# Optimization experiments

Measured on AMD Instinct MI355X. Metric: run time of the kernel, lower is better.

Reference implementation:

```python
import jax, jax.numpy as jnp
import numpy as np

H = 768
L = 4096
P, KP = 8192, 8
EV, KE = 2048, 6
E = 16384
NR = 32
NUM_LABELS = 2


def setup_inputs() -> dict:
    key = jax.random.key(0)
    ks = jax.random.split(key, 10)
    seq = jax.random.normal(ks[0], (1, L, H), dtype=jnp.float32)
    phrase_idx = jax.random.randint(ks[1], (P, KP), 0, L, dtype=jnp.int32)
    phrase_mask = jnp.ones((P, KP), dtype=jnp.float32)
    event_idx = jax.random.randint(ks[2], (EV, KE), 0, L, dtype=jnp.int32)
    event_mask = jnp.ones((EV, KE), dtype=jnp.float32)
    pair_idx = jax.random.randint(ks[3], (E, 2), 0, EV, dtype=jnp.int32)
    root_idx = jax.random.randint(ks[4], (NR,), 0, P, dtype=jnp.int32)
    s1 = 1.0 / np.sqrt(2 * H)
    W1 = jax.random.normal(ks[5], (2 * H, H), dtype=jnp.float32) * s1
    b1 = jnp.zeros((H,), dtype=jnp.float32)
    Wb = jax.random.normal(ks[6], (2 * H, NUM_LABELS), dtype=jnp.float32) * s1
    bb = jnp.zeros((NUM_LABELS,), dtype=jnp.float32)
    return {"seq": seq, "phrase_idx": phrase_idx, "phrase_mask": phrase_mask,
            "event_idx": event_idx, "event_mask": event_mask, "pair_idx": pair_idx,
            "root_idx": root_idx, "W1": W1, "b1": b1, "Wb": Wb, "bb": bb}


def _masked_mean_gather(tok, idx, mask):
    # tok: [L,H]; idx: [N,K] int; mask: [N,K] float -> [N,H]
    g = tok[idx]                                  # [N,K,H] irregular gather
    s = jnp.einsum('nkh,nk->nh', g, mask)
    d = jnp.maximum(mask.sum(axis=1, keepdims=True), 1.0)
    return s / d


def reference(seq, phrase_idx, phrase_mask, event_idx, event_mask, pair_idx,
              root_idx, W1, b1, Wb, bb):
    tok = seq[0]                                   # [L,H] doc token embeddings
    # phrase embeddings: gather token indices per phrase, masked mean-pool
    ph = _masked_mean_gather(tok, phrase_idx, phrase_mask)   # [P,H]
    # event embeddings: gather span tokens per event, masked mean-pool
    ev = _masked_mean_gather(tok, event_idx, event_mask)     # [EV,H]
    # event-pair nodes: concat the two event embeddings, middle_layer MLP
    e1 = ev[pair_idx[:, 0]]                        # [E,H]
    e2 = ev[pair_idx[:, 1]]                        # [E,H]
    pairs = jnp.concatenate([e1, e2], axis=-1)     # [E,2H]
    node = jax.nn.relu(pairs @ W1 + b1)            # [E,H] (dropout inactive at eval)
    # virtual root: mean of sentence-root phrase embeddings
    vroot = ph[root_idx].mean(axis=0)              # [H]
    feat = jnp.concatenate([node, jnp.broadcast_to(vroot, node.shape)], axis=-1)
    logits = feat @ Wb + bb                        # [E,NUM_LABELS] bilinear classifier
    return logits
```

## Files before the change

### kernel.cpp

```cpp
#include <hip/hip_runtime.h>
#include <hip/hip_bf16.h>

#define H   768
#define H4  192
#define EVN 2048
#define KE  6
#define KP  8
#define EE  16384
#define NR  32

typedef __bf16 v8bf __attribute__((ext_vector_type(8)));
typedef float  v4f  __attribute__((ext_vector_type(4)));

__device__ __forceinline__ void gload16(const void* g, void* lds) {
    __builtin_amdgcn_global_load_lds(
        (const __attribute__((address_space(1))) void*)g,
        (__attribute__((address_space(3))) void*)lds, 16, 0, 0);
}
__device__ __forceinline__ float blo(unsigned u) {
    return __uint_as_float(u << 16);
}
__device__ __forceinline__ float bhi(unsigned u) {
    return __uint_as_float(u & 0xffff0000u);
}

__global__ __launch_bounds__(256) void pre_kernel(
    const float* __restrict__ seq,
    const int* __restrict__ eidx, const float* __restrict__ emask,
    const int* __restrict__ pidx, const float* __restrict__ pmask,
    const int* __restrict__ root_idx, const float* __restrict__ W1,
    const float* __restrict__ Wb,
    __hip_bfloat16* __restrict__ evb, __hip_bfloat16* __restrict__ Wt,
    float* __restrict__ dotr) {
    __shared__ float tile[64][65];
    const int b = blockIdx.x;
    const int t = threadIdx.x;
    const float4* seq4 = (const float4*)seq;

    if (b < 512) {
        const int w = t >> 6, l = t & 63;
        const int n = b * 4 + w;
        int idx[KE]; float mk[KE]; float ms = 0.f;
#pragma unroll
        for (int k = 0; k < KE; ++k) {
            idx[k] = eidx[n * KE + k];
            mk[k]  = emask[n * KE + k];
            ms    += mk[k];
        }
        const float inv = 1.f / fmaxf(ms, 1.f);
#pragma unroll
        for (int g = 0; g < 3; ++g) {
            const int t4 = l + g * 64;
            float4 acc = {0.f, 0.f, 0.f, 0.f};
#pragma unroll
            for (int k = 0; k < KE; ++k) {
                float4 v = seq4[idx[k] * H4 + t4];
                acc.x = fmaf(mk[k], v.x, acc.x);
                acc.y = fmaf(mk[k], v.y, acc.y);
                acc.z = fmaf(mk[k], v.z, acc.z);
                acc.w = fmaf(mk[k], v.w, acc.w);
            }
            __hip_bfloat16 o[4];
            o[0] = __float2bfloat16(acc.x * inv);
            o[1] = __float2bfloat16(acc.y * inv);
            o[2] = __float2bfloat16(acc.z * inv);
            o[3] = __float2bfloat16(acc.w * inv);
            *(uint2*)&evb[n * H + t4 * 4] = *(uint2*)o;
        }
    } else if (b < 520) {
        const int w = t >> 6, l = t & 63;
        const int r = (b - 512) * 4 + w;
        const int pr = root_idx[r];
        int idx[KP]; float mk[KP]; float ms = 0.f;
#pragma unroll
        for (int k = 0; k < KP; ++k) {
            idx[k] = pidx[pr * KP + k];
            mk[k]  = pmask[pr * KP + k];
            ms    += mk[k];
        }
        const float inv = 1.f / fmaxf(ms, 1.f);
        float p0 = 0.f, p1 = 0.f;
#pragma unroll
        for (int g = 0; g < 3; ++g) {
            const int t4 = l + g * 64;
            float4 a = {0.f, 0.f, 0.f, 0.f};
#pragma unroll
            for (int k = 0; k < KP; ++k) {
                float4 v = seq4[idx[k] * H4 + t4];
                a.x = fmaf(mk[k], v.x, a.x);
                a.y = fmaf(mk[k], v.y, a.y);
                a.z = fmaf(mk[k], v.z, a.z);
                a.w = fmaf(mk[k], v.w, a.w);
            }
            const int d = t4 * 4;
            float4 q0 = *(const float4*)&Wb[(H + d) * 2];
            float4 q1 = *(const float4*)&Wb[(H + d) * 2 + 4];
            p0 += inv * (a.x * q0.x + a.y * q0.z + a.z * q1.x + a.w * q1.z);
            p1 += inv * (a.x * q0.y + a.y * q0.w + a.z * q1.y + a.w * q1.w);
        }
#pragma unroll
        for (int off = 32; off > 0; off >>= 1) {
            p0 += __shfl_xor(p0, off, 64);
            p1 += __shfl_xor(p1, off, 64);
        }
        if (l == 0) {
            dotr[r * 2 + 0] = p0 * (1.0f / NR);
            dotr[r * 2 + 1] = p1 * (1.0f / NR);
        }
    } else {
        const int b2 = b - 520;
        const int k0 = (b2 % 12) * 64;
        const int j0 = (b2 / 12) * 64;
        const int s  = (j0 >= H) ? H : 0;
        const int n0 = j0 - s;
        const int c  = t & 63;
        const int r0 = t >> 6;
#pragma unroll
        for (int i = 0; i < 16; ++i) {
            const int r = r0 + i * 4;
            tile[r][c] = W1[(size_t)(s + k0 + r) * H + n0 + c];
        }
        __syncthreads();
#pragma unroll
        for (int i = 0; i < 16; ++i) {
            const int r = r0 + i * 4;
            Wt[(size_t)(j0 + r) * H + k0 + c] = __float2bfloat16(tile[c][r]);
        }
    }
}

__global__ __launch_bounds__(256) void gemm_kernel(
    const __hip_bfloat16* __restrict__ evb_,
    const __hip_bfloat16* __restrict__ Wt_,
    const float* __restrict__ b1v,
    __hip_bfloat16* __restrict__ evw) {
    __shared__ short As[3][8192];
    __shared__ short Bs[3][6144];

    const short* evb = (const short*)evb_;
    const short* Wt  = (const short*)Wt_;

    const int bid = blockIdx.x;
    const int swz = (bid & 7) * 32 + (bid >> 3);
    const int mt = swz >> 4, nt = swz & 15;
    const int m0 = mt * 128, n0 = nt * 96;

    const int t = threadIdx.x;
    const int l = t & 63;
    const int w = t >> 6;
    const int wr = (w >> 1) * 64;
    const int wc = (w & 1) * 48;

    const short* aSrc[4]; int aOff[4];
#pragma unroll
    for (int c = 0; c < 4; ++c) {
        const int s = c * 256 + t;
        const int r = s >> 3, pg = s & 7, g = pg ^ (r & 7);
        aSrc[c] = evb + (size_t)(m0 + r) * H + g * 8;
        aOff[c] = s * 16;
    }
    const short* bSrc[3]; int bOff[3];
#pragma unroll
    for (int c = 0; c < 3; ++c) {
        const int s = c * 256 + t;
        const int r = s >> 3, pg = s & 7, g = pg ^ (r & 7);
        bSrc[c] = Wt + (size_t)(n0 + r) * H + g * 8;
        bOff[c] = s * 16;
    }

#define STAGE(tile, buf) do {                                              \
    _Pragma("unroll") for (int c_ = 0; c_ < 4; ++c_)                       \
        gload16(aSrc[c_] + (tile) * 64, (char*)As[buf] + aOff[c_]);        \
    _Pragma("unroll") for (int c_ = 0; c_ < 3; ++c_)                       \
        gload16(bSrc[c_] + (tile) * 64, (char*)Bs[buf] + bOff[c_]);        \
} while (0)

    const int fr = l & 15, gq = l >> 4, xm = fr & 7;
    int aRowB[4], bRowB[3];
#pragma unroll
    for (int mi = 0; mi < 4; ++mi) aRowB[mi] = (wr + mi * 16 + fr) * 128;
#pragma unroll
    for (int nj = 0; nj < 3; ++nj) bRowB[nj] = (wc + nj * 16 + fr) * 128;

    v4f acc[4][3] = {};

    STAGE(0, 0);
    STAGE(1, 1);

#pragma unroll
    for (int ks = 0; ks < 12; ++ks) {
        if (ks < 11) { asm volatile("s_waitcnt vmcnt(7)" ::: "memory"); }
        else         { asm volatile("s_waitcnt vmcnt(0)" ::: "memory"); }
        __builtin_amdgcn_sched_barrier(0);
        __builtin_amdgcn_s_barrier();
        __builtin_amdgcn_sched_barrier(0);
        if (ks < 10) STAGE(ks + 2, (ks + 2) % 3);
        const char* Ab = (const char*)As[ks % 3];
        const char* Bb = (const char*)Bs[ks % 3];
#pragma unroll
        for (int hh = 0; hh < 2; ++hh) {
            const int pgo = ((hh * 4 + gq) ^ xm) * 16;
            v8bf a0 = *(const v8bf*)(Ab + aRowB[0] + pgo);
            v8bf a1 = *(const v8bf*)(Ab + aRowB[1] + pgo);
            v8bf a2 = *(const v8bf*)(Ab + aRowB[2] + pgo);
            v8bf a3 = *(const v8bf*)(Ab + aRowB[3] + pgo);
            v8bf b0 = *(const v8bf*)(Bb + bRowB[0] + pgo);
            v8bf b1 = *(const v8bf*)(Bb + bRowB[1] + pgo);
            v8bf b2 = *(const v8bf*)(Bb + bRowB[2] + pgo);
            acc[0][0] = __builtin_amdgcn_mfma_f32_16x16x32_bf16(a0, b0, acc[0][0], 0, 0, 0);
            acc[0][1] = __builtin_amdgcn_mfma_f32_16x16x32_bf16(a0, b1, acc[0][1], 0, 0, 0);
            acc[0][2] = __builtin_amdgcn_mfma_f32_16x16x32_bf16(a0, b2, acc[0][2], 0, 0, 0);
            acc[1][0] = __builtin_amdgcn_mfma_f32_16x16x32_bf16(a1, b0, acc[1][0], 0, 0, 0);
            acc[1][1] = __builtin_amdgcn_mfma_f32_16x16x32_bf16(a1, b1, acc[1][1], 0, 0, 0);
            acc[1][2] = __builtin_amdgcn_mfma_f32_16x16x32_bf16(a1, b2, acc[1][2], 0, 0, 0);
            acc[2][0] = __builtin_amdgcn_mfma_f32_16x16x32_bf16(a2, b0, acc[2][0], 0, 0, 0);
            acc[2][1] = __builtin_amdgcn_mfma_f32_16x16x32_bf16(a2, b1, acc[2][1], 0, 0, 0);
            acc[2][2] = __builtin_amdgcn_mfma_f32_16x16x32_bf16(a2, b2, acc[2][2], 0, 0, 0);
            acc[3][0] = __builtin_amdgcn_mfma_f32_16x16x32_bf16(a3, b0, acc[3][0], 0, 0, 0);
            acc[3][1] = __builtin_amdgcn_mfma_f32_16x16x32_bf16(a3, b1, acc[3][1], 0, 0, 0);
            acc[3][2] = __builtin_amdgcn_mfma_f32_16x16x32_bf16(a3, b2, acc[3][2], 0, 0, 0);
        }
    }
#undef STAGE

    float bv[3];
#pragma unroll
    for (int nj = 0; nj < 3; ++nj) {
        const int ocol = n0 + wc + nj * 16 + fr;
        bv[nj] = (ocol >= H) ? b1v[ocol - H] : 0.f;
    }
#pragma unroll
    for (int mi = 0; mi < 4; ++mi)
#pragma unroll
        for (int nj = 0; nj < 3; ++nj) {
            const int ocol = n0 + wc + nj * 16 + fr;
#pragma unroll
            for (int r = 0; r < 4; ++r) {
                const int orow = m0 + wr + mi * 16 + gq * 4 + r;
                evw[(size_t)orow * 1536 + ocol] =
                    __float2bfloat16(acc[mi][nj][r] + bv[nj]);
            }
        }
}

__global__ __launch_bounds__(256) void pair_logits_kernel(
    const __hip_bfloat16* __restrict__ evw_, const int* __restrict__ pair_idx,
    const float* __restrict__ Wb, const float* __restrict__ dotr,
    const float* __restrict__ bbv, float* __restrict__ out) {
    const ushort* evw = (const ushort*)evw_;
    const int wave = threadIdx.x >> 6;
    const int lane = threadIdx.x & 63;

    float c0 = 0.f, c1 = 0.f;
    if (lane < 32) { c0 = dotr[lane * 2]; c1 = dotr[lane * 2 + 1]; }
#pragma unroll
    for (int off = 32; off > 0; off >>= 1) {
        c0 += __shfl_xor(c0, off, 64);
        c1 += __shfl_xor(c1, off, 64);
    }
    c0 += bbv[0]; c1 += bbv[1];

    const int i = blockIdx.x * 4 + wave;
    const int p0 = pair_idx[i * 2 + 0];
    const int p1 = pair_idx[i * 2 + 1];
    const ushort* ra = evw + (size_t)p0 * 1536;
    const ushort* rb = evw + (size_t)p1 * 1536 + H;
    float acc0 = 0.f, acc1 = 0.f;
#pragma unroll
    for (int h = 0; h < 2; ++h) {
        const int j = h * 384 + lane * 6;
        uint3 ua = *(const uint3*)(ra + j);
        uint3 ub = *(const uint3*)(rb + j);
        float4 w0 = *(const float4*)(Wb + j * 2);
        float4 w1 = *(const float4*)(Wb + j * 2 + 4);
        float4 w2 = *(const float4*)(Wb + j * 2 + 8);
        float n0 = fmaxf(blo(ua.x) + blo(ub.x), 0.f);
        float n1 = fmaxf(bhi(ua.x) + bhi(ub.x), 0.f);
        float n2 = fmaxf(blo(ua.y) + blo(ub.y), 0.f);
        float n3 = fmaxf(bhi(ua.y) + bhi(ub.y), 0.f);
        float n4 = fmaxf(blo(ua.z) + blo(ub.z), 0.f);
        float n5 = fmaxf(bhi(ua.z) + bhi(ub.z), 0.f);
        acc0 += n0 * w0.x + n1 * w0.z + n2 * w1.x + n3 * w1.z + n4 * w2.x + n5 * w2.z;
        acc1 += n0 * w0.y + n1 * w0.w + n2 * w1.y + n3 * w1.w + n4 * w2.y + n5 * w2.w;
    }
#pragma unroll
    for (int off = 32; off > 0; off >>= 1) {
        acc0 += __shfl_xor(acc0, off, 64);
        acc1 += __shfl_xor(acc1, off, 64);
    }
    if (lane == 0) {
        out[i * 2 + 0] = acc0 + c0;
        out[i * 2 + 1] = acc1 + c1;
    }
}

extern "C" void kernel_launch(void* const* d_in, const int* in_sizes, int n_in,
                              void* d_out, int out_size, void* d_ws, size_t ws_size,
                              hipStream_t stream) {
    const float* seq         = (const float*)d_in[0];
    const int*   phrase_idx  = (const int*)  d_in[1];
    const float* phrase_mask = (const float*)d_in[2];
    const int*   event_idx   = (const int*)  d_in[3];
    const float* event_mask  = (const float*)d_in[4];
    const int*   pair_idx    = (const int*)  d_in[5];
    const int*   root_idx    = (const int*)  d_in[6];
    const float* W1          = (const float*)d_in[7];
    const float* b1          = (const float*)d_in[8];
    const float* Wb          = (const float*)d_in[9];
    const float* bb          = (const float*)d_in[10];
    float* out = (float*)d_out;

    char* wsb = (char*)d_ws;
    __hip_bfloat16* evb = (__hip_bfloat16*)wsb;
    __hip_bfloat16* Wt  = (__hip_bfloat16*)(wsb + 3145728);
    __hip_bfloat16* evw = (__hip_bfloat16*)(wsb + 5505024);
    float* dotr = (float*)(wsb + 11796480);

    pre_kernel<<<808, 256, 0, stream>>>(seq, event_idx, event_mask,
                                        phrase_idx, phrase_mask, root_idx,
                                        W1, Wb, evb, Wt, dotr);
    gemm_kernel<<<256, 256, 0, stream>>>(evb, Wt, b1, evw);
    pair_logits_kernel<<<EE / 4, 256, 0, stream>>>(evw, pair_idx, Wb, dotr,
                                                   bb, out);
}
```

Before: 33.89 us.

## Load GEMM B operand directly to registers and shrink N tile to 64

The GEMM stops staging the weight tile through LDS. Each wave now loads its B fragments straight from global memory into double-buffered registers one k-step ahead. The N tile drops from 96 to 64 columns, so the grid grows from 256 to 384 blocks with a new swizzle, and the vmcnt wait counts are adjusted to match. This removes LDS traffic and shared memory for B and raises block count for better CU coverage, at the cost of uncoalesced, redundant per-wave global reads of B and less reuse of A per block.

```diff
diff --git a/kernel.cpp b/kernel.cpp
--- a/kernel.cpp
+++ b/kernel.cpp
@@ -135,21 +135,20 @@
     const float* __restrict__ b1v,
     __hip_bfloat16* __restrict__ evw) {
     __shared__ short As[3][8192];
-    __shared__ short Bs[3][6144];
 
     const short* evb = (const short*)evb_;
     const short* Wt  = (const short*)Wt_;
 
     const int bid = blockIdx.x;
-    const int swz = (bid & 7) * 32 + (bid >> 3);
-    const int mt = swz >> 4, nt = swz & 15;
-    const int m0 = mt * 128, n0 = nt * 96;
+    const int swz = (bid & 7) * 48 + (bid >> 3);
+    const int mt = swz / 24, nt = swz % 24;
+    const int m0 = mt * 128, n0 = nt * 64;
 
     const int t = threadIdx.x;
     const int l = t & 63;
     const int w = t >> 6;
     const int wr = (w >> 1) * 64;
-    const int wc = (w & 1) * 48;
+    const int wc = (w & 1) * 32;
 
     const short* aSrc[4]; int aOff[4];
 #pragma unroll
@@ -159,44 +158,53 @@
         aSrc[c] = evb + (size_t)(m0 + r) * H + g * 8;
         aOff[c] = s * 16;
     }
-    const short* bSrc[3]; int bOff[3];
-#pragma unroll
-    for (int c = 0; c < 3; ++c) {
-        const int s = c * 256 + t;
-        const int r = s >> 3, pg = s & 7, g = pg ^ (r & 7);
-        bSrc[c] = Wt + (size_t)(n0 + r) * H + g * 8;
-        bOff[c] = s * 16;
-    }
-
-#define STAGE(tile, buf) do {                                              \
+
+#define STAGEA(tile, buf) do {                                             \
     _Pragma("unroll") for (int c_ = 0; c_ < 4; ++c_)                       \
         gload16(aSrc[c_] + (tile) * 64, (char*)As[buf] + aOff[c_]);        \
-    _Pragma("unroll") for (int c_ = 0; c_ < 3; ++c_)                       \
-        gload16(bSrc[c_] + (tile) * 64, (char*)Bs[buf] + bOff[c_]);        \
 } while (0)
 
     const int fr = l & 15, gq = l >> 4, xm = fr & 7;
-    int aRowB[4], bRowB[3];
+    int aRowB[4];
 #pragma unroll
     for (int mi = 0; mi < 4; ++mi) aRowB[mi] = (wr + mi * 16 + fr) * 128;
-#pragma unroll
-    for (int nj = 0; nj < 3; ++nj) bRowB[nj] = (wc + nj * 16 + fr) * 128;
-
-    v4f acc[4][3] = {};
-
-    STAGE(0, 0);
-    STAGE(1, 1);
+
+    const short* bPtr[2];
+#pragma unroll
+    for (int nj = 0; nj < 2; ++nj)
+        bPtr[nj] = Wt + (size_t)(n0 + wc + nj * 16 + fr) * H + gq * 8;
+
+    v8bf bS0[2][2], bS1[2][2];
+
+#define LOADB0(ks) do {                                                    \
+    _Pragma("unroll") for (int nj_ = 0; nj_ < 2; ++nj_)                    \
+        _Pragma("unroll") for (int hh_ = 0; hh_ < 2; ++hh_)                \
+            bS0[nj_][hh_] =                                                \
+                *(const v8bf*)(bPtr[nj_] + (ks) * 64 + hh_ * 32);          \
+} while (0)
+#define LOADB1(ks) do {                                                    \
+    _Pragma("unroll") for (int nj_ = 0; nj_ < 2; ++nj_)                    \
+        _Pragma("unroll") for (int hh_ = 0; hh_ < 2; ++hh_)                \
+            bS1[nj_][hh_] =                                                \
+                *(const v8bf*)(bPtr[nj_] + (ks) * 64 + hh_ * 32);          \
+} while (0)
+
+    v4f acc[4][2] = {};
+
+    LOADB0(0);
+    STAGEA(0, 0);
+    STAGEA(1, 1);
 
 #pragma unroll
     for (int ks = 0; ks < 12; ++ks) {
-        if (ks < 11) { asm volatile("s_waitcnt vmcnt(7)" ::: "memory"); }
+        if (ks < 11) { asm volatile("s_waitcnt vmcnt(4)" ::: "memory"); }
         else         { asm volatile("s_waitcnt vmcnt(0)" ::: "memory"); }
         __builtin_amdgcn_sched_barrier(0);
         __builtin_amdgcn_s_barrier();
         __builtin_amdgcn_sched_barrier(0);
-        if (ks < 10) STAGE(ks + 2, (ks + 2) % 3);
+        if (ks < 11) { if (ks & 1) LOADB0(ks + 1); else LOADB1(ks + 1); }
+        if (ks < 10) STAGEA(ks + 2, (ks + 2) % 3);
         const char* Ab = (const char*)As[ks % 3];
-        const char* Bb = (const char*)Bs[ks % 3];
 #pragma unroll
         for (int hh = 0; hh < 2; ++hh) {
             const int pgo = ((hh * 4 + gq) ^ xm) * 16;
@@ -204,35 +212,32 @@
             v8bf a1 = *(const v8bf*)(Ab + aRowB[1] + pgo);
             v8bf a2 = *(const v8bf*)(Ab + aRowB[2] + pgo);
             v8bf a3 = *(const v8bf*)(Ab + aRowB[3] + pgo);
-            v8bf b0 = *(const v8bf*)(Bb + bRowB[0] + pgo);
-            v8bf b1 = *(const v8bf*)(Bb + bRowB[1] + pgo);
-            v8bf b2 = *(const v8bf*)(Bb + bRowB[2] + pgo);
+            v8bf b0 = (ks & 1) ? bS1[0][hh] : bS0[0][hh];
+            v8bf b1 = (ks & 1) ? bS1[1][hh] : bS0[1][hh];
             acc[0][0] = __builtin_amdgcn_mfma_f32_16x16x32_bf16(a0, b0, acc[0][0], 0, 0, 0);
             acc[0][1] = __builtin_amdgcn_mfma_f32_16x16x32_bf16(a0, b1, acc[0][1], 0, 0, 0);
-            acc[0][2] = __builtin_amdgcn_mfma_f32_16x16x32_bf16(a0, b2, acc[0][2], 0, 0, 0);
             acc[1][0] = __builtin_amdgcn_mfma_f32_16x16x32_bf16(a1, b0, acc[1][0], 0, 0, 0);
             acc[1][1] = __builtin_amdgcn_mfma_f32_16x16x32_bf16(a1, b1, acc[1][1], 0, 0, 0);
-            acc[1][2] = __builtin_amdgcn_mfma_f32_16x16x32_bf16(a1, b2, acc[1][2], 0, 0, 0);
             acc[2][0] = __builtin_amdgcn_mfma_f32_16x16x32_bf16(a2, b0, acc[2][0], 0, 0, 0);
             acc[2][1] = __builtin_amdgcn_mfma_f32_16x16x32_bf16(a2, b1, acc[2][1], 0, 0, 0);
-            acc[2][2] = __builtin_amdgcn_mfma_f32_16x16x32_bf16(a2, b2, acc[2][2], 0, 0, 0);
             acc[3][0] = __builtin_amdgcn_mfma_f32_16x16x32_bf16(a3, b0, acc[3][0], 0, 0, 0);
             acc[3][1] = __builtin_amdgcn_mfma_f32_16x16x32_bf16(a3, b1, acc[3][1], 0, 0, 0);
-            acc[3][2] = __builtin_amdgcn_mfma_f32_16x16x32_bf16(a3, b2, acc[3][2], 0, 0, 0);
-        }
-    }
-#undef STAGE
-
-    float bv[3];
-#pragma unroll
-    for (int nj = 0; nj < 3; ++nj) {
+        }
+    }
+#undef STAGEA
+#undef LOADB0
+#undef LOADB1
+
+    float bv[2];
+#pragma unroll
+    for (int nj = 0; nj < 2; ++nj) {
         const int ocol = n0 + wc + nj * 16 + fr;
         bv[nj] = (ocol >= H) ? b1v[ocol - H] : 0.f;
     }
 #pragma unroll
     for (int mi = 0; mi < 4; ++mi)
 #pragma unroll
-        for (int nj = 0; nj < 3; ++nj) {
+        for (int nj = 0; nj < 2; ++nj) {
             const int ocol = n0 + wc + nj * 16 + fr;
 #pragma unroll
             for (int r = 0; r < 4; ++r) {
@@ -319,7 +324,7 @@
     pre_kernel<<<808, 256, 0, stream>>>(seq, event_idx, event_mask,
                                         phrase_idx, phrase_mask, root_idx,
                                         W1, Wb, evb, Wt, dotr);
-    gemm_kernel<<<256, 256, 0, stream>>>(evb, Wt, b1, evw);
+    gemm_kernel<<<384, 256, 0, stream>>>(evb, Wt, b1, evw);
     pair_logits_kernel<<<EE / 4, 256, 0, stream>>>(evw, pair_idx, Wb, dotr,
                                                    bb, out);
 }
```

Result: slower. 39.74 us (+17.2%).
